# Optimization experiments

Hardware: AMD Instinct MI355X
Metric: run time of the kernel (lower is better)

Reference implementation:

```python
import jax, jax.numpy as jnp
import numpy as np

IN_F = 4096
OUT_F = 4096
BLOCK = 8
N_CENTROIDS = 2048
N_BLOCKS = IN_F // BLOCK  # 512
N_TOKENS = 1024


def setup_inputs() -> dict:
    key = jax.random.key(0)
    k1, k2, k3, k4 = jax.random.split(key, 4)
    x = jax.random.normal(k1, (N_TOKENS, IN_F), dtype=jnp.float32)
    centroids = jax.random.normal(k2, (N_CENTROIDS, BLOCK), dtype=jnp.float32)
    # assignments: block-major layout, length n_blocks * out_features
    assignments = jax.random.randint(k3, (N_BLOCKS * OUT_F,), 0, N_CENTROIDS, dtype=jnp.int32)
    bias = jax.random.normal(k4, (OUT_F,), dtype=jnp.float32) * 0.01
    # counts = bincount(assignments), used only in backward (grad averaging)
    counts = jax.ops.segment_sum(
        jnp.ones_like(assignments, dtype=jnp.float32), assignments,
        num_segments=N_CENTROIDS)
    return {"x": x, "centroids": centroids, "bias": bias,
            "assignments": assignments, "counts": counts}


def reference(x, centroids, bias, assignments, counts):
    # weight = centroids[assignments].reshape(n_blocks, out_f, block)
    #                        .permute(1,0,2).reshape(out_f, in_f)
    w = centroids[assignments]  # [n_blocks*out_f, block]
    w = w.reshape(N_BLOCKS, OUT_F, BLOCK).transpose(1, 0, 2).reshape(OUT_F, IN_F)
    # F.linear(x, weight, bias) = x @ w.T + bias
    return x @ w.T + bias
```

## Files before the change

### kernel.cpp

```cpp
#include <hip/hip_runtime.h>
#include <hip/hip_bf16.h>

#define IN_F   4096
#define OUT_F  4096
#define QBLK   8
#define NBLKS  512
#define NTOK   1024
#define NCENT  2048

typedef unsigned int u32;
typedef unsigned short u16;
typedef __attribute__((ext_vector_type(8))) short short8;
typedef __attribute__((ext_vector_type(4))) float floatx4;

__device__ __forceinline__ u16 f2bf(float f) {
  union { float f; u32 u; } v; v.f = f;
  u32 u = v.u;
  return (u16)((u + 0x7fffu + ((u >> 16) & 1u)) >> 16);
}

__device__ __forceinline__ void load_lds_16(const void* g, void* l) {
  __builtin_amdgcn_global_load_lds(
      (const __attribute__((address_space(1))) u32*)g,
      (__attribute__((address_space(3))) u32*)l, 16, 0, 0);
}

__global__ __launch_bounds__(256) void cast_bf16_kernel(
    const float* __restrict__ src, u16* __restrict__ dst) {
  int g = blockIdx.x * 256 + threadIdx.x;
  const float4* sv = (const float4*)src;
  float4 a = sv[(size_t)g * 2];
  float4 b = sv[(size_t)g * 2 + 1];
  union { u16 s[8]; uint4 v; } o;
  o.s[0] = f2bf(a.x); o.s[1] = f2bf(a.y); o.s[2] = f2bf(a.z); o.s[3] = f2bf(a.w);
  o.s[4] = f2bf(b.x); o.s[5] = f2bf(b.y); o.s[6] = f2bf(b.z); o.s[7] = f2bf(b.w);
  ((uint4*)dst)[g] = o.v;
}

__global__ __launch_bounds__(256) void cast_swz_kernel(
    const float* __restrict__ src, u16* __restrict__ dst) {
  __shared__ __align__(16) u16 ls[256 * 8];
  const int b = blockIdx.x;
  const int mg = b >> 5;
  const int kq = b & 31;
  const int t = threadIdx.x;
  const int ml = t >> 4;
  const int kbl = t & 15;

  const float* p = src + (size_t)(mg * 16 + ml) * IN_F + kq * 128 + kbl * 8;
  float4 a = ((const float4*)p)[0];
  float4 c = ((const float4*)p)[1];
  union { u16 s[8]; uint4 v; } o;
  o.s[0] = f2bf(a.x); o.s[1] = f2bf(a.y); o.s[2] = f2bf(a.z); o.s[3] = f2bf(a.w);
  o.s[4] = f2bf(c.x); o.s[5] = f2bf(c.y); o.s[6] = f2bf(c.z); o.s[7] = f2bf(c.w);

  const int cidx = (kbl << 4) | (ml ^ kbl);
  *(uint4*)&ls[cidx * 8] = o.v;
  __syncthreads();

  const int g = (t & 0xF0) | ((t & 15) ^ ((t >> 4) & 15));
  uint4* dbase = (uint4*)(dst + (size_t)(mg * 512 + kq * 16) * 128);
  dbase[g] = ((const uint4*)ls)[t];
}

__global__ __launch_bounds__(256, 3) void gemm_fused_kernel(
    const u16* __restrict__ xs,
    const u16* __restrict__ centb,
    const int* __restrict__ assign,
    const float* __restrict__ bias,
    float* __restrict__ out0,
    float* __restrict__ partials) {
  __shared__ __align__(16) u16 cs[NCENT * 8];

  const int t = threadIdx.x;
  const int lane = t & 63;
  const int wv = t >> 6;
  const int wm = wv >> 1;
  const int wn = wv & 1;
  const int quad = lane >> 4;
  const int r16 = lane & 15;
  const int m0 = blockIdx.y * 128;
  const int n0 = blockIdx.x * 128;
  const int s = blockIdx.z;
  const int kchunk = IN_F / gridDim.z;
  const int kb0 = (s * kchunk) >> 3;
  const int iters = kchunk / 32;

#pragma unroll
  for (int it = 0; it < 8; ++it) {
    int c = it * 256 + t;
    load_lds_16(centb + (size_t)c * 8, cs + (size_t)c * 8);
  }

  floatx4 acc[4][4];
#pragma unroll
  for (int i = 0; i < 4; ++i)
#pragma unroll
    for (int j = 0; j < 4; ++j)
#pragma unroll
      for (int r = 0; r < 4; ++r) acc[i][j][r] = 0.0f;

  const int ncol = n0 + wn * 64 + r16;
  const short8* xv = (const short8*)xs;
  const short8* csv = (const short8*)cs;

  const int mgrp0 = (m0 >> 4) + wm * 4;
  size_t abase[4];
#pragma unroll
  for (int i = 0; i < 4; ++i)
    abase[i] = ((size_t)(mgrp0 + i) * 512 + kb0 + quad) * 16 + r16;

  const int* aptr = assign + (size_t)(kb0 + quad) * OUT_F + ncol;

  short8 afc[4];
#pragma unroll
  for (int i = 0; i < 4; ++i) afc[i] = xv[abase[i]];
  int idxc[4];
#pragma unroll
  for (int j = 0; j < 4; ++j) idxc[j] = aptr[j * 16];

  __syncthreads();

  for (int kt = 0; kt < iters; ++kt) {
    short8 afn[4];
    int idxn[4];
    if (kt + 1 < iters) {
#pragma unroll
      for (int i = 0; i < 4; ++i) afn[i] = xv[abase[i] + (size_t)(kt + 1) * 64];
#pragma unroll
      for (int j = 0; j < 4; ++j) idxn[j] = aptr[(size_t)(kt + 1) * 4 * OUT_F + j * 16];
    }

    short8 bfr[4];
#pragma unroll
    for (int j = 0; j < 4; ++j) bfr[j] = csv[idxc[j]];

    __builtin_amdgcn_s_setprio(1);
#pragma unroll
    for (int i = 0; i < 4; ++i)
#pragma unroll
      for (int j = 0; j < 4; ++j)
        acc[i][j] = __builtin_amdgcn_mfma_f32_16x16x32_bf16(afc[i], bfr[j], acc[i][j], 0, 0, 0);
    __builtin_amdgcn_s_setprio(0);

#pragma unroll
    for (int i = 0; i < 4; ++i) afc[i] = afn[i];
#pragma unroll
    for (int j = 0; j < 4; ++j) idxc[j] = idxn[j];
  }

  float* C = (s == 0) ? out0 : (partials + (size_t)(s - 1) * NTOK * OUT_F);
  const bool add_bias = (gridDim.z == 1);
  const int row_base = m0 + wm * 64 + quad * 4;
#pragma unroll
  for (int j = 0; j < 4; ++j) {
    const int col = ncol + j * 16;
    const float bv = add_bias ? bias[col] : 0.0f;
#pragma unroll
    for (int i = 0; i < 4; ++i) {
      const int row = row_base + i * 16;
#pragma unroll
      for (int r = 0; r < 4; ++r)
        C[(size_t)(row + r) * OUT_F + col] = acc[i][j][r] + bv;
    }
  }
}

__global__ __launch_bounds__(256) void reduce_kernel(
    float* __restrict__ out, const float* __restrict__ partials,
    const float* __restrict__ bias, int sm1) {
  int g = blockIdx.x * 256 + threadIdx.x;
  float4 v = ((const float4*)out)[g];
  for (int s = 0; s < sm1; ++s) {
    float4 p = ((const float4*)(partials + (size_t)s * NTOK * OUT_F))[g];
    v.x += p.x; v.y += p.y; v.z += p.z; v.w += p.w;
  }
  float4 b = ((const float4*)bias)[g & (OUT_F / 4 - 1)];
  v.x += b.x; v.y += b.y; v.z += b.z; v.w += b.w;
  ((float4*)out)[g] = v;
}

extern "C" void kernel_launch(void* const* d_in, const int* in_sizes, int n_in,
                              void* d_out, int out_size, void* d_ws, size_t ws_size,
                              hipStream_t stream) {
  const float* x      = (const float*)d_in[0];
  const float* cent   = (const float*)d_in[1];
  const float* bias   = (const float*)d_in[2];
  const int*   assign = (const int*)d_in[3];
  float* out = (float*)d_out;

  const size_t xb_bytes   = (size_t)NTOK * IN_F * sizeof(u16);
  const size_t cent_bytes = (size_t)NCENT * 8 * sizeof(u16);
  const size_t part_bytes = (size_t)NTOK * OUT_F * sizeof(float);
  u16*   xs       = (u16*)d_ws;
  u16*   centb    = (u16*)((char*)d_ws + xb_bytes);
  float* partials = (float*)((char*)d_ws + xb_bytes + cent_bytes);

  const size_t base = xb_bytes + cent_bytes;
  int S = 1;
  if (ws_size >= base + 3 * part_bytes) S = 4;
  else if (ws_size >= base + 1 * part_bytes) S = 2;

  hipLaunchKernelGGL(cast_swz_kernel, dim3(64 * 32), dim3(256), 0, stream, x, xs);
  hipLaunchKernelGGL(cast_bf16_kernel, dim3((NCENT * 8 / 8) / 256), dim3(256), 0, stream,
                     cent, centb);
  hipLaunchKernelGGL(gemm_fused_kernel, dim3(OUT_F / 128, NTOK / 128, S), dim3(256), 0, stream,
                     xs, centb, assign, bias, out, partials);
  if (S > 1)
    hipLaunchKernelGGL(reduce_kernel, dim3((NTOK * OUT_F / 4) / 256), dim3(256), 0, stream,
                       out, partials, bias, S - 1);
}
```

Baseline: 136.7 us.

## Replace split-K partial buffers and reduce kernel with atomic accumulation

```diff
diff --git a/kernel.cpp b/kernel.cpp
--- a/kernel.cpp
+++ b/kernel.cpp
@@ -7,6 +7,10 @@
 #define NBLKS  512
 #define NTOK   1024
 #define NCENT  2048
+
+#define SPLITK 4
+#define KCHUNK (IN_F / SPLITK)
+#define KITERS (KCHUNK / 32)
 
 typedef unsigned int u32;
 typedef unsigned short u16;
@@ -23,6 +27,11 @@
   __builtin_amdgcn_global_load_lds(
       (const __attribute__((address_space(1))) u32*)g,
       (__attribute__((address_space(3))) u32*)l, 16, 0, 0);
+}
+
+__global__ __launch_bounds__(256) void zero_kernel(float* __restrict__ p) {
+  int g = blockIdx.x * 256 + threadIdx.x;
+  ((float4*)p)[g] = make_float4(0.f, 0.f, 0.f, 0.f);
 }
 
 __global__ __launch_bounds__(256) void cast_bf16_kernel(
@@ -63,13 +72,12 @@
   dbase[g] = ((const uint4*)ls)[t];
 }
 
-__global__ __launch_bounds__(256, 3) void gemm_fused_kernel(
+__global__ __launch_bounds__(256, 4) void gemm_fused_kernel(
     const u16* __restrict__ xs,
     const u16* __restrict__ centb,
     const int* __restrict__ assign,
     const float* __restrict__ bias,
-    float* __restrict__ out0,
-    float* __restrict__ partials) {
+    float* __restrict__ out) {
   __shared__ __align__(16) u16 cs[NCENT * 8];
 
   const int t = threadIdx.x;
@@ -82,9 +90,7 @@
   const int m0 = blockIdx.y * 128;
   const int n0 = blockIdx.x * 128;
   const int s = blockIdx.z;
-  const int kchunk = IN_F / gridDim.z;
-  const int kb0 = (s * kchunk) >> 3;
-  const int iters = kchunk / 32;
+  const int kb0 = (s * KCHUNK) >> 3;
 
 #pragma unroll
   for (int it = 0; it < 8; ++it) {
@@ -101,47 +107,47 @@
       for (int r = 0; r < 4; ++r) acc[i][j][r] = 0.0f;
 
   const int ncol = n0 + wn * 64 + r16;
-  const short8* xv = (const short8*)xs;
-  const short8* csv = (const short8*)cs;
 
-  const int mgrp0 = (m0 >> 4) + wm * 4;
-  size_t abase[4];
+  const char* xA = (const char*)xs +
+      ((size_t)((m0 >> 4) + wm * 4) * 512 + kb0) * 256;
+  const u32 va = (u32)(quad * 256 + r16 * 16);
+  const int* ai = assign + (size_t)kb0 * OUT_F;
+  const u32 vi = (u32)(quad * OUT_F + ncol);
+
+  short8 afc[4];
+  int idxc[4];
 #pragma unroll
   for (int i = 0; i < 4; ++i)
-    abase[i] = ((size_t)(mgrp0 + i) * 512 + kb0 + quad) * 16 + r16;
-
-  const int* aptr = assign + (size_t)(kb0 + quad) * OUT_F + ncol;
-
-  short8 afc[4];
+    afc[i] = *(const short8*)(xA + (va + (u32)i * 131072u));
 #pragma unroll
-  for (int i = 0; i < 4; ++i) afc[i] = xv[abase[i]];
-  int idxc[4];
-#pragma unroll
-  for (int j = 0; j < 4; ++j) idxc[j] = aptr[j * 16];
+  for (int j = 0; j < 4; ++j) idxc[j] = ai[vi + (u32)(j * 16)];
 
   __syncthreads();
 
-  for (int kt = 0; kt < iters; ++kt) {
+  const short8* csv = (const short8*)cs;
+#pragma unroll 2
+  for (int kt = 0; kt < KITERS; ++kt) {
     short8 afn[4];
     int idxn[4];
-    if (kt + 1 < iters) {
+    if (kt + 1 < KITERS) {
+      const char* xk = xA + (va + (u32)((kt + 1) * 1024));
 #pragma unroll
-      for (int i = 0; i < 4; ++i) afn[i] = xv[abase[i] + (size_t)(kt + 1) * 64];
+      for (int i = 0; i < 4; ++i)
+        afn[i] = *(const short8*)(xk + (u32)i * 131072u);
+      const int* an = ai + (size_t)(kt + 1) * 4 * OUT_F;
 #pragma unroll
-      for (int j = 0; j < 4; ++j) idxn[j] = aptr[(size_t)(kt + 1) * 4 * OUT_F + j * 16];
+      for (int j = 0; j < 4; ++j) idxn[j] = an[vi + (u32)(j * 16)];
     }
 
     short8 bfr[4];
 #pragma unroll
     for (int j = 0; j < 4; ++j) bfr[j] = csv[idxc[j]];
 
-    __builtin_amdgcn_s_setprio(1);
 #pragma unroll
     for (int i = 0; i < 4; ++i)
 #pragma unroll
       for (int j = 0; j < 4; ++j)
         acc[i][j] = __builtin_amdgcn_mfma_f32_16x16x32_bf16(afc[i], bfr[j], acc[i][j], 0, 0, 0);
-    __builtin_amdgcn_s_setprio(0);
 
 #pragma unroll
     for (int i = 0; i < 4; ++i) afc[i] = afn[i];
@@ -149,35 +155,19 @@
     for (int j = 0; j < 4; ++j) idxc[j] = idxn[j];
   }
 
-  float* C = (s == 0) ? out0 : (partials + (size_t)(s - 1) * NTOK * OUT_F);
-  const bool add_bias = (gridDim.z == 1);
   const int row_base = m0 + wm * 64 + quad * 4;
 #pragma unroll
   for (int j = 0; j < 4; ++j) {
     const int col = ncol + j * 16;
-    const float bv = add_bias ? bias[col] : 0.0f;
+    const float bv = (s == 0) ? bias[col] : 0.0f;
 #pragma unroll
     for (int i = 0; i < 4; ++i) {
       const int row = row_base + i * 16;
 #pragma unroll
       for (int r = 0; r < 4; ++r)
-        C[(size_t)(row + r) * OUT_F + col] = acc[i][j][r] + bv;
+        unsafeAtomicAdd(&out[(size_t)(row + r) * OUT_F + col], acc[i][j][r] + bv);
     }
   }
-}
-
-__global__ __launch_bounds__(256) void reduce_kernel(
-    float* __restrict__ out, const float* __restrict__ partials,
-    const float* __restrict__ bias, int sm1) {
-  int g = blockIdx.x * 256 + threadIdx.x;
-  float4 v = ((const float4*)out)[g];
-  for (int s = 0; s < sm1; ++s) {
-    float4 p = ((const float4*)(partials + (size_t)s * NTOK * OUT_F))[g];
-    v.x += p.x; v.y += p.y; v.z += p.z; v.w += p.w;
-  }
-  float4 b = ((const float4*)bias)[g & (OUT_F / 4 - 1)];
-  v.x += b.x; v.y += b.y; v.z += b.z; v.w += b.w;
-  ((float4*)out)[g] = v;
 }
 
 extern "C" void kernel_launch(void* const* d_in, const int* in_sizes, int n_in,
@@ -189,24 +179,14 @@
   const int*   assign = (const int*)d_in[3];
   float* out = (float*)d_out;
 
-  const size_t xb_bytes   = (size_t)NTOK * IN_F * sizeof(u16);
-  const size_t cent_bytes = (size_t)NCENT * 8 * sizeof(u16);
-  const size_t part_bytes = (size_t)NTOK * OUT_F * sizeof(float);
-  u16*   xs       = (u16*)d_ws;
-  u16*   centb    = (u16*)((char*)d_ws + xb_bytes);
-  float* partials = (float*)((char*)d_ws + xb_bytes + cent_bytes);
+  const size_t xb_bytes = (size_t)NTOK * IN_F * sizeof(u16);
+  u16* xs    = (u16*)d_ws;
+  u16* centb = (u16*)((char*)d_ws + xb_bytes);
 
-  const size_t base = xb_bytes + cent_bytes;
-  int S = 1;
-  if (ws_size >= base + 3 * part_bytes) S = 4;
-  else if (ws_size >= base + 1 * part_bytes) S = 2;
-
+  hipLaunchKernelGGL(zero_kernel, dim3((NTOK * OUT_F / 4) / 256), dim3(256), 0, stream, out);
   hipLaunchKernelGGL(cast_swz_kernel, dim3(64 * 32), dim3(256), 0, stream, x, xs);
   hipLaunchKernelGGL(cast_bf16_kernel, dim3((NCENT * 8 / 8) / 256), dim3(256), 0, stream,
                      cent, centb);
-  hipLaunchKernelGGL(gemm_fused_kernel, dim3(OUT_F / 128, NTOK / 128, S), dim3(256), 0, stream,
-                     xs, centb, assign, bias, out, partials);
-  if (S > 1)
-    hipLaunchKernelGGL(reduce_kernel, dim3((NTOK * OUT_F / 4) / 256), dim3(256), 0, stream,
-                       out, partials, bias, S - 1);
+  hipLaunchKernelGGL(gemm_fused_kernel, dim3(OUT_F / 128, NTOK / 128, SPLITK), dim3(256), 0, stream,
+                     xs, centb, assign, bias, out);
 }
```

Result: slower. 158.7 us (+16.1%).
